# Performance work log

Measured on AMD Instinct MI355X. Metric: run time of the kernel, lower is better.

The kernel has to match this reference:

```python
import jax, jax.numpy as jnp
import numpy as np

B, S, IN, HID, HEADS, TRAITS = 128, 32, 32, 128, 8, 10


def setup_inputs() -> dict:
    key = jax.random.key(0)
    ks = jax.random.split(key, 40)
    f32 = jnp.float32
    def W(k, shape, s=0.02):
        return (jax.random.normal(k, shape, f32) * s)
    path = jax.random.normal(ks[0], (B, S, IN), f32)
    # monotonically increasing shared time grid (timestamps[0] is what cdeint uses)
    dt = jax.random.uniform(ks[1], (S,), f32, 0.05, 0.15)
    ts = jnp.broadcast_to(jnp.cumsum(dt), (B, S))
    inp = {
        "interaction_path": path,
        "timestamps": ts,
        # initial encoder: Linear(IN,HID) -> LN -> GELU -> Linear(HID,HID) -> LN
        "enc_W1": W(ks[2], (IN, HID)), "enc_b1": jnp.zeros((HID,), f32),
        "enc_g1": jnp.ones((HID,), f32), "enc_bt1": jnp.zeros((HID,), f32),
        "enc_W2": W(ks[3], (HID, HID)), "enc_b2": jnp.zeros((HID,), f32),
        "enc_g2": jnp.ones((HID,), f32), "enc_bt2": jnp.zeros((HID,), f32),
        # vector field: Linear(HID,2HID)->LN->GELU -> Linear(2HID,2HID)->LN->GELU -> Linear(2HID,HID*IN)
        "vf_W1": W(ks[4], (HID, 2 * HID)), "vf_b1": jnp.zeros((2 * HID,), f32),
        "vf_g1": jnp.ones((2 * HID,), f32), "vf_bt1": jnp.zeros((2 * HID,), f32),
        "vf_W2": W(ks[5], (2 * HID, 2 * HID)), "vf_b2": jnp.zeros((2 * HID,), f32),
        "vf_g2": jnp.ones((2 * HID,), f32), "vf_bt2": jnp.zeros((2 * HID,), f32),
        "vf_W3": W(ks[6], (2 * HID, HID * IN), 0.005), "vf_b3": jnp.zeros((HID * IN,), f32),
        # MultiheadAttention (q=k=v, single token)
        "Wq": W(ks[7], (HID, HID)), "bq": jnp.zeros((HID,), f32),
        "Wk": W(ks[8], (HID, HID)), "bk": jnp.zeros((HID,), f32),
        "Wv": W(ks[9], (HID, HID)), "bv": jnp.zeros((HID,), f32),
        "Wo": W(ks[10], (HID, HID)), "bo": jnp.zeros((HID,), f32),
        # trait decoder (2-layer MLP -> TRAITS)
        "dec_W1": W(ks[11], (HID, HID)), "dec_b1": jnp.zeros((HID,), f32),
        "dec_W2": W(ks[12], (HID, TRAITS)), "dec_b2": jnp.zeros((TRAITS,), f32),
    }
    return inp


def reference(interaction_path, timestamps,
              enc_W1, enc_b1, enc_g1, enc_bt1, enc_W2, enc_b2, enc_g2, enc_bt2,
              vf_W1, vf_b1, vf_g1, vf_bt1, vf_W2, vf_b2, vf_g2, vf_bt2, vf_W3, vf_b3,
              Wq, bq, Wk, bk, Wv, bv, Wo, bo,
              dec_W1, dec_b1, dec_W2, dec_b2):
    b, s, in_dim = interaction_path.shape
    hid = enc_W1.shape[1]
    nh = HEADS
    dh = hid // nh

    def ln(x, g, bb):
        mu = jnp.mean(x, -1, keepdims=True)
        v = jnp.mean((x - mu) ** 2, -1, keepdims=True)
        return (x - mu) / jnp.sqrt(v + 1e-5) * g + bb

    gelu = lambda x: jax.nn.gelu(x, approximate=False)

    # initial encoder on first time point (dropout = eval mode)
    x0 = interaction_path[:, 0]
    h0 = gelu(ln(x0 @ enc_W1 + enc_b1, enc_g1, enc_bt1))
    z0 = ln(h0 @ enc_W2 + enc_b2, enc_g2, enc_bt2)  # [B, HID]

    # linear-interpolation control path: piecewise-constant derivative per interval
    dts = timestamps[:, 1:] - timestamps[:, :-1]                       # [B, S-1]
    dX = (interaction_path[:, 1:] - interaction_path[:, :-1]) / dts[..., None]  # [B, S-1, IN]

    def vf(z):
        h = gelu(ln(z @ vf_W1 + vf_b1, vf_g1, vf_bt1))
        h = gelu(ln(h @ vf_W2 + vf_b2, vf_g2, vf_bt2))
        return (h @ vf_W3 + vf_b3).reshape(z.shape[0], hid, in_dim)    # [B, HID, IN]

    def drift(z, dxdt):
        return jnp.einsum('bhi,bi->bh', vf(z), dxdt)

    def rk4_step(z, inp):
        dxdt, hstep = inp               # [B, IN], [B]
        hb = hstep[:, None]
        k1 = drift(z, dxdt)
        k2 = drift(z + 0.5 * hb * k1, dxdt)
        k3 = drift(z + 0.5 * hb * k2, dxdt)
        k4 = drift(z + hb * k3, dxdt)
        z_next = z + (hb / 6.0) * (k1 + 2 * k2 + 2 * k3 + k4)
        return z_next, None

    zT, _ = jax.lax.scan(rk4_step, z0, (jnp.swapaxes(dX, 0, 1), dts.T))  # [B, HID]

    # single-token self-attention (softmax over one key -> weights = 1)
    q = (zT @ Wq + bq).reshape(b, nh, dh)
    k = (zT @ Wk + bk).reshape(b, nh, dh)
    v = (zT @ Wv + bv).reshape(b, nh, dh)
    scores = jnp.sum(q * k, -1, keepdims=True) / jnp.sqrt(jnp.float32(dh))  # [B, nh, 1]
    w = jax.nn.softmax(scores[..., None], axis=-1)                           # [B, nh, 1, 1] == 1
    attn = (w[..., 0] * v).reshape(b, hid)
    final = attn @ Wo + bo
    attention_weights = jnp.mean(w, axis=1)  # [B, 1, 1] averaged over heads (torch default)

    hD = gelu(final @ dec_W1 + dec_b1)
    traits = hD @ dec_W2 + dec_b2            # [B, TRAITS]
    return traits, attention_weights
```

## Files before the change

kernel.cpp:

```cpp
#include <hip/hip_runtime.h>
#include <hip/hip_bf16.h>

#define BB 128
#define SS 32
#define NSTEP 31
#define IND 32
#define HID 128
#define HID2 256

typedef unsigned short u16;
typedef unsigned int u32;
typedef _Float16 f16;
typedef f16 h2 __attribute__((ext_vector_type(2)));
typedef __fp16 fp16v2 __attribute__((ext_vector_type(2)));
typedef _Float16 f16x8 __attribute__((ext_vector_type(8)));
typedef float f32x4 __attribute__((ext_vector_type(4)));

__device__ __forceinline__ float dot2f(u32 a, u32 b, float c){
#if __has_builtin(__builtin_amdgcn_fdot2)
  h2 ha, hb; __builtin_memcpy(&ha, &a, 4); __builtin_memcpy(&hb, &b, 4);
  return __builtin_amdgcn_fdot2(ha, hb, c, false);
#else
  h2 ha, hb; __builtin_memcpy(&ha, &a, 4); __builtin_memcpy(&hb, &b, 4);
  return c + (float)ha[0]*(float)hb[0] + (float)ha[1]*(float)hb[1];
#endif
}
__device__ __forceinline__ u32 pkh2(float a, float b){
  fp16v2 r = __builtin_amdgcn_cvt_pkrtz(a, b);
  u32 u; __builtin_memcpy(&u, &r, 4); return u;
}
__device__ __forceinline__ u16 f2h(float f){ f16 h = (f16)f; u16 u; __builtin_memcpy(&u, &h, 2); return u; }
__device__ __forceinline__ float gelu_f(float x){ return 0.5f * x * (1.0f + erff(x * 0.70710678118654752440f)); }

__device__ __forceinline__ float wred(float v){
  int iv; float tf;
  #define DPPADD(CTRL, RMASK) \
    __builtin_memcpy(&iv, &v, 4); \
    iv = __builtin_amdgcn_update_dpp(0, iv, CTRL, RMASK, 0xf, true); \
    __builtin_memcpy(&tf, &iv, 4); \
    v += tf;
  DPPADD(0x111, 0xf)
  DPPADD(0x112, 0xf)
  DPPADD(0x114, 0xf)
  DPPADD(0x118, 0xf)
  DPPADD(0x142, 0xa)
  DPPADD(0x143, 0xc)
  #undef DPPADD
  return v;
}

__device__ __forceinline__ void bsum2(float x, float y, float* red, int tid, float& ox, float& oy){
  #pragma unroll
  for (int off = 32; off >= 1; off >>= 1){ x += __shfl_xor(x, off); y += __shfl_xor(y, off); }
  __syncthreads();
  if ((tid & 63) == 0){ red[(tid >> 6)*2] = x; red[(tid >> 6)*2 + 1] = y; }
  __syncthreads();
  ox = red[0] + red[2] + red[4] + red[6];
  oy = red[1] + red[3] + red[5] + red[7];
}

__global__ __launch_bounds__(128) void prep_misc(const float* __restrict__ path,
                                                 const float* __restrict__ ts,
                                                 const float* __restrict__ b3,
                                                 u32* __restrict__ dxh,
                                                 float* __restrict__ hb,
                                                 float* __restrict__ gb){
  const int b = blockIdx.x, tid = threadIdx.x;
  __shared__ float sdx[NSTEP * IND];
  for (int t = tid; t < NSTEP * IND; t += 128){
    int s = t >> 5, i = t & 31;
    float dt = ts[b*SS + s + 1] - ts[b*SS + s];
    sdx[t] = (path[(b*SS + s + 1)*IND + i] - path[(b*SS + s)*IND + i]) / dt;
  }
  if (tid < NSTEP) hb[b*NSTEP + tid] = ts[b*SS + tid + 1] - ts[b*SS + tid];
  __syncthreads();
  for (int t = tid; t < NSTEP * 16; t += 128){
    int s = t >> 4, i2 = t & 15;
    dxh[((size_t)b*NSTEP + s)*16 + i2] = pkh2(sdx[s*IND + 2*i2], sdx[s*IND + 2*i2 + 1]);
  }
  if (tid < HID){
    float w[IND];
    #pragma unroll
    for (int i = 0; i < IND; ++i) w[i] = b3[tid*IND + i];
    for (int s = 0; s < NSTEP; ++s){
      float a = 0.f;
      #pragma unroll
      for (int i = 0; i < IND; ++i) a = fmaf(w[i], sdx[s*IND + i], a);
      gb[(b*NSTEP + s)*HID + tid] = a;
    }
  }
}

__global__ __launch_bounds__(256) void pack_w3(const float* __restrict__ W3, u32* __restrict__ w3h){
  int i = blockIdx.x*256 + threadIdx.x;
  if (i < (HID2*HID*IND)/2) w3h[i] = pkh2(W3[2*i], W3[2*i + 1]);
}

__global__ __launch_bounds__(256) void pack_wf(const float* __restrict__ W1,
                                               const float* __restrict__ W2,
                                               u32* __restrict__ w1f,
                                               u32* __restrict__ w2f){
  int i = blockIdx.x*256 + threadIdx.x;
  if (i < 16384){
    int lane_blk = i >> 6, rem = i & 63;
    int i16 = rem >> 2, q = rem & 3;
    int w = lane_blk >> 6, lane = lane_blk & 63;
    int kt = i16 >> 2, nt = i16 & 3;
    int k = kt*32 + (lane >> 4)*8 + 2*q;
    int col = w*64 + nt*16 + (lane & 15);
    w1f[i] = pkh2(W1[(size_t)k*HID2 + col], W1[(size_t)(k+1)*HID2 + col]);
  } else if (i < 16384 + 32768){
    int j = i - 16384;
    int lane_blk = j >> 7, rem = j & 127;
    int i32i = rem >> 2, q = rem & 3;
    int w = lane_blk >> 6, lane = lane_blk & 63;
    int kt = i32i >> 2, nt = i32i & 3;
    int k = kt*32 + (lane >> 4)*8 + 2*q;
    int col = w*64 + nt*16 + (lane & 15);
    w2f[j] = pkh2(W2[(size_t)k*HID2 + col], W2[(size_t)(k+1)*HID2 + col]);
  }
}

__global__ __launch_bounds__(256) void gprep_h(const u32* __restrict__ w3h,
                                               const u32* __restrict__ dxh,
                                               u32* __restrict__ Gp, int s0){
  const int tid = threadIdx.x;
  const int sl = blockIdx.y; const int s = s0 + sl;
  const int lin = blockIdx.x*256 + tid;
  const int kp = lin >> 7, h = lin & 127;
  const uint4* wa = (const uint4*)(w3h + ((size_t)(2*kp)*HID + h)*16);
  const uint4* wb = (const uint4*)(w3h + ((size_t)(2*kp+1)*HID + h)*16);
  uint4 A0 = wa[0], A1 = wa[1], A2 = wa[2], A3 = wa[3];
  uint4 B0 = wb[0], B1 = wb[1], B2 = wb[2], B3 = wb[3];
  __shared__ u32 sdx[BB * 16];
  for (int t = tid; t < BB * 16; t += 256){
    int bb = t >> 4, i2 = t & 15;
    sdx[t] = dxh[((size_t)bb*NSTEP + s)*16 + i2];
  }
  __syncthreads();
  const int kt = kp >> 4, q = kp & 3, quad2 = (kp >> 2) & 3;
  const int wq = h >> 5, tq = (h >> 4) & 1, nn = h & 15;
  const size_t off = (size_t)wq*4096 + (size_t)(kt*2 + tq)*256 + (size_t)(quad2*16 + nn)*4 + q;
  const size_t base_sl = (size_t)sl * BB * 16384;
  for (int bb = 0; bb < BB; ++bb){
    const uint4* dp = (const uint4*)&sdx[bb*16];
    uint4 D0 = dp[0], D1 = dp[1], D2 = dp[2], D3 = dp[3];
    float g0 = 0.f, g1 = 0.f, g2 = 0.f, g3 = 0.f;
    g0 = dot2f(D0.x, A0.x, g0); g0 = dot2f(D0.y, A0.y, g0);
    g0 = dot2f(D0.z, A0.z, g0); g0 = dot2f(D0.w, A0.w, g0);
    g2 = dot2f(D1.x, A1.x, g2); g2 = dot2f(D1.y, A1.y, g2);
    g2 = dot2f(D1.z, A1.z, g2); g2 = dot2f(D1.w, A1.w, g2);
    g0 = dot2f(D2.x, A2.x, g0); g0 = dot2f(D2.y, A2.y, g0);
    g0 = dot2f(D2.z, A2.z, g0); g0 = dot2f(D2.w, A2.w, g0);
    g2 = dot2f(D3.x, A3.x, g2); g2 = dot2f(D3.y, A3.y, g2);
    g2 = dot2f(D3.z, A3.z, g2); g2 = dot2f(D3.w, A3.w, g2);
    g1 = dot2f(D0.x, B0.x, g1); g1 = dot2f(D0.y, B0.y, g1);
    g1 = dot2f(D0.z, B0.z, g1); g1 = dot2f(D0.w, B0.w, g1);
    g3 = dot2f(D1.x, B1.x, g3); g3 = dot2f(D1.y, B1.y, g3);
    g3 = dot2f(D1.z, B1.z, g3); g3 = dot2f(D1.w, B1.w, g3);
    g1 = dot2f(D2.x, B2.x, g1); g1 = dot2f(D2.y, B2.y, g1);
    g1 = dot2f(D2.z, B2.z, g1); g1 = dot2f(D2.w, B2.w, g1);
    g3 = dot2f(D3.x, B3.x, g3); g3 = dot2f(D3.y, B3.y, g3);
    g3 = dot2f(D3.z, B3.z, g3); g3 = dot2f(D3.w, B3.w, g3);
    Gp[base_sl + (size_t)bb*16384 + off] = pkh2(g0 + g2, g1 + g3);
  }
}

struct ScanP {
  const float *path;
  const float *eW1,*eb1,*eg1,*ebt1,*eW2,*eb2,*eg2,*ebt2;
  const u32 *w1f, *w2f;
  const float *b1,*g1,*bt1,*b2,*g2,*bt2;
  const float *Wv,*bv,*Wo,*bo,*dW1,*db1,*dW2,*db2;
  const float *hb,*gb;
  const u32 *Gp;
  float *zstate, *out;
  int s0, s1, do_enc, do_epi;
};

__global__ __launch_bounds__(256, 1) void scan_kernel(ScanP p){
  const int tid = threadIdx.x;
  const int b = blockIdx.x;
  const int lane = tid & 63, w = tid >> 6;
  const int quad = lane >> 4, n16 = lane & 15;
  const bool owner = (quad == 0);
  __shared__ __align__(16) u16 zst_h[HID];
  __shared__ __align__(16) u16 a1p_h[HID2];
  __shared__ __align__(16) u16 a2p_h[HID2];
  __shared__ __align__(16) float red[8];
  __shared__ __align__(16) float zf[HID];
  __shared__ __align__(16) float sc1[HID2];

  uint4 w1r[16], w2r[32];
  {
    const uint4* s1p = (const uint4*)p.w1f + ((size_t)(w*64 + lane))*16;
    #pragma unroll
    for (int i = 0; i < 16; ++i) w1r[i] = s1p[i];
    const uint4* s2p = (const uint4*)p.w2f + ((size_t)(w*64 + lane))*32;
    #pragma unroll
    for (int i = 0; i < 32; ++i) w2r[i] = s2p[i];
  }
  float rb1[4], rg1[4], rbt1[4], rb2[4], rg2[4], rbt2[4];
  #pragma unroll
  for (int nt = 0; nt < 4; ++nt){
    int col = w*64 + nt*16 + n16;
    rb1[nt] = p.b1[col]; rg1[nt] = p.g1[col]; rbt1[nt] = p.bt1[col];
    rb2[nt] = p.b2[col]; rg2[nt] = p.g2[col]; rbt2[nt] = p.bt2[col];
  }
  const int h0 = w*32 + n16, h1 = h0 + 16;

  float mu, sq;
  if (p.do_enc){
    if (tid < IND) sc1[tid] = p.path[(b*SS + 0)*IND + tid];
    __syncthreads();
    float acc = 0.f;
    if (tid < HID){
      acc = p.eb1[tid];
      #pragma unroll 8
      for (int i = 0; i < IND; ++i) acc = fmaf(sc1[i], p.eW1[i*HID + tid], acc);
    }
    float cx = (tid < HID) ? acc : 0.f;
    bsum2(cx, cx*cx, red, tid, mu, sq);
    mu *= (1.f/HID); float var = sq*(1.f/HID) - mu*mu; float rstd = rsqrtf(var + 1e-5f);
    if (tid < HID) zf[tid] = gelu_f((acc - mu)*rstd*p.eg1[tid] + p.ebt1[tid]);
    __syncthreads();
    float acc2 = 0.f;
    if (tid < HID){
      acc2 = p.eb2[tid];
      #pragma unroll 8
      for (int h = 0; h < HID; ++h) acc2 = fmaf(zf[h], p.eW2[h*HID + tid], acc2);
    }
    cx = (tid < HID) ? acc2 : 0.f;
    bsum2(cx, cx*cx, red, tid, mu, sq);
    mu *= (1.f/HID); float var2 = sq*(1.f/HID) - mu*mu; float rstd2 = rsqrtf(var2 + 1e-5f);
    __syncthreads();
    if (tid < HID) zf[tid] = (acc2 - mu)*rstd2*p.eg2[tid] + p.ebt2[tid];
    __syncthreads();
  }
  float zc0 = 0.f, zc1 = 0.f;
  if (owner){
    if (p.do_enc){ zc0 = zf[h0]; zc1 = zf[h1]; }
    else { zc0 = p.zstate[b*HID + h0]; zc1 = p.zstate[b*HID + h1]; }
  }

  for (int s = p.s0; s < p.s1; ++s){
    const float hbv = p.hb[b*NSTEP + s];
    uint4 gr[16];
    {
      const uint4* g4 = (const uint4*)(p.Gp + ((size_t)(s - p.s0)*BB + b)*16384 + (size_t)w*4096);
      #pragma unroll
      for (int m = 0; m < 16; ++m) gr[m] = g4[m*64 + lane];
    }
    float gb0 = 0.f, gb1 = 0.f;
    if (owner){
      gb0 = p.gb[(b*NSTEP + s)*HID + h0];
      gb1 = p.gb[(b*NSTEP + s)*HID + h1];
      zst_h[h0] = f2h(zc0); zst_h[h1] = f2h(zc1);
    }
    float ks0 = 0.f, ks1 = 0.f;
    __syncthreads();

    #pragma unroll 1
    for (int st = 0; st < 4; ++st){
      f32x4 D0 = {0,0,0,0}, D1 = {0,0,0,0}, D2 = {0,0,0,0}, D3 = {0,0,0,0};
      {
        const uint4* za = (const uint4*)zst_h;
        #pragma unroll
        for (int kt = 0; kt < 4; ++kt){
          f16x8 a; uint4 av = za[kt*4 + quad]; __builtin_memcpy(&a, &av, 16);
          f16x8 bf;
          __builtin_memcpy(&bf, &w1r[kt*4+0], 16); D0 = __builtin_amdgcn_mfma_f32_16x16x32_f16(a, bf, D0, 0, 0, 0);
          __builtin_memcpy(&bf, &w1r[kt*4+1], 16); D1 = __builtin_amdgcn_mfma_f32_16x16x32_f16(a, bf, D1, 0, 0, 0);
          __builtin_memcpy(&bf, &w1r[kt*4+2], 16); D2 = __builtin_amdgcn_mfma_f32_16x16x32_f16(a, bf, D2, 0, 0, 0);
          __builtin_memcpy(&bf, &w1r[kt*4+3], 16); D3 = __builtin_amdgcn_mfma_f32_16x16x32_f16(a, bf, D3, 0, 0, 0);
        }
      }
      float v0 = D0[0] + rb1[0], v1 = D1[0] + rb1[1], v2 = D2[0] + rb1[2], v3 = D3[0] + rb1[3];
      float ssum = wred((v0 + v1) + (v2 + v3));
      float ssq  = wred((v0*v0 + v1*v1) + (v2*v2 + v3*v3));
      if (lane == 63){ red[w*2] = ssum; red[w*2+1] = ssq; }
      __syncthreads();
      {
        const float4* r4 = (const float4*)red;
        float4 ra = r4[0], rb = r4[1];
        float m1 = (ra.x + ra.z + rb.x + rb.z)*(1.f/1024.f);
        float q1 = (ra.y + ra.w + rb.y + rb.w)*(1.f/1024.f);
        float rs1 = rsqrtf(q1 - m1*m1 + 1e-5f);
        if (owner){
          a1p_h[w*64 +  0 + n16] = f2h(gelu_f((v0 - m1)*rs1*rg1[0] + rbt1[0]));
          a1p_h[w*64 + 16 + n16] = f2h(gelu_f((v1 - m1)*rs1*rg1[1] + rbt1[1]));
          a1p_h[w*64 + 32 + n16] = f2h(gelu_f((v2 - m1)*rs1*rg1[2] + rbt1[2]));
          a1p_h[w*64 + 48 + n16] = f2h(gelu_f((v3 - m1)*rs1*rg1[3] + rbt1[3]));
        }
      }
      __syncthreads();
      D0 = {0,0,0,0}; D1 = {0,0,0,0}; D2 = {0,0,0,0}; D3 = {0,0,0,0};
      {
        const uint4* aa = (const uint4*)a1p_h;
        #pragma unroll
        for (int kt = 0; kt < 8; ++kt){
          f16x8 a; uint4 av = aa[kt*4 + quad]; __builtin_memcpy(&a, &av, 16);
          f16x8 bf;
          __builtin_memcpy(&bf, &w2r[kt*4+0], 16); D0 = __builtin_amdgcn_mfma_f32_16x16x32_f16(a, bf, D0, 0, 0, 0);
          __builtin_memcpy(&bf, &w2r[kt*4+1], 16); D1 = __builtin_amdgcn_mfma_f32_16x16x32_f16(a, bf, D1, 0, 0, 0);
          __builtin_memcpy(&bf, &w2r[kt*4+2], 16); D2 = __builtin_amdgcn_mfma_f32_16x16x32_f16(a, bf, D2, 0, 0, 0);
          __builtin_memcpy(&bf, &w2r[kt*4+3], 16); D3 = __builtin_amdgcn_mfma_f32_16x16x32_f16(a, bf, D3, 0, 0, 0);
        }
      }
      v0 = D0[0] + rb2[0]; v1 = D1[0] + rb2[1]; v2 = D2[0] + rb2[2]; v3 = D3[0] + rb2[3];
      ssum = wred((v0 + v1) + (v2 + v3));
      ssq  = wred((v0*v0 + v1*v1) + (v2*v2 + v3*v3));
      if (lane == 63){ red[w*2] = ssum; red[w*2+1] = ssq; }
      __syncthreads();
      {
        const float4* r4 = (const float4*)red;
        float4 ra = r4[0], rb = r4[1];
        float m2 = (ra.x + ra.z + rb.x + rb.z)*(1.f/1024.f);
        float q2 = (ra.y + ra.w + rb.y + rb.w)*(1.f/1024.f);
        float rs2 = rsqrtf(q2 - m2*m2 + 1e-5f);
        if (owner){
          a2p_h[w*64 +  0 + n16] = f2h(gelu_f((v0 - m2)*rs2*rg2[0] + rbt2[0]));
          a2p_h[w*64 + 16 + n16] = f2h(gelu_f((v1 - m2)*rs2*rg2[1] + rbt2[1]));
          a2p_h[w*64 + 32 + n16] = f2h(gelu_f((v2 - m2)*rs2*rg2[2] + rbt2[2]));
          a2p_h[w*64 + 48 + n16] = f2h(gelu_f((v3 - m2)*rs2*rg2[3] + rbt2[3]));
        }
      }
      __syncthreads();
      f32x4 E0 = {0,0,0,0}, E1 = {0,0,0,0};
      {
        const uint4* aa = (const uint4*)a2p_h;
        #pragma unroll
        for (int kt = 0; kt < 8; ++kt){
          f16x8 a; uint4 av = aa[kt*4 + quad]; __builtin_memcpy(&a, &av, 16);
          f16x8 g0f, g1f;
          __builtin_memcpy(&g0f, &gr[kt*2+0], 16);
          __builtin_memcpy(&g1f, &gr[kt*2+1], 16);
          E0 = __builtin_amdgcn_mfma_f32_16x16x32_f16(a, g0f, E0, 0, 0, 0);
          E1 = __builtin_amdgcn_mfma_f32_16x16x32_f16(a, g1f, E1, 0, 0, 0);
        }
      }
      if (owner){
        float kv0 = E0[0] + gb0, kv1 = E1[0] + gb1;
        float cst = (st == 0 || st == 3) ? 1.f : 2.f;
        ks0 += cst*kv0; ks1 += cst*kv1;
        if (st < 3){
          float c = (st == 2) ? hbv : 0.5f*hbv;
          zst_h[h0] = f2h(zc0 + c*kv0);
          zst_h[h1] = f2h(zc1 + c*kv1);
        }
      }
      __syncthreads();
    }
    if (owner){ zc0 += hbv*(1.f/6.f)*ks0; zc1 += hbv*(1.f/6.f)*ks1; }
  }

  if (p.do_epi){
    if (owner){ zf[h0] = zc0; zf[h1] = zc1; }
    __syncthreads();
    if (tid < HID){
      float v = p.bv[tid];
      #pragma unroll 8
      for (int h = 0; h < HID; ++h) v = fmaf(zf[h], p.Wv[h*HID + tid], v);
      sc1[tid] = v;
    }
    __syncthreads();
    if (tid < HID){
      float f = p.bo[tid];
      #pragma unroll 8
      for (int h = 0; h < HID; ++h) f = fmaf(sc1[h], p.Wo[h*HID + tid], f);
      sc1[HID + tid] = f;
    }
    __syncthreads();
    if (tid < HID){
      float hd = p.db1[tid];
      #pragma unroll 8
      for (int h = 0; h < HID; ++h) hd = fmaf(sc1[HID + h], p.dW1[h*HID + tid], hd);
      zf[tid] = gelu_f(hd);
    }
    __syncthreads();
    if (tid < 10){
      float t = p.db2[tid];
      #pragma unroll 8
      for (int h = 0; h < HID; ++h) t = fmaf(zf[h], p.dW2[h*10 + tid], t);
      p.out[b*10 + tid] = t;
    }
    if (tid == 0) p.out[BB*10 + b] = 1.0f;
  } else {
    if (owner){ p.zstate[b*HID + h0] = zc0; p.zstate[b*HID + h1] = zc1; }
  }
}

extern "C" void kernel_launch(void* const* d_in, const int* in_sizes, int n_in,
                              void* d_out, int out_size, void* d_ws, size_t ws_size,
                              hipStream_t stream){
  const float* path  = (const float*)d_in[0];
  const float* ts    = (const float*)d_in[1];
  const float* eW1   = (const float*)d_in[2];
  const float* eb1   = (const float*)d_in[3];
  const float* eg1   = (const float*)d_in[4];
  const float* ebt1  = (const float*)d_in[5];
  const float* eW2   = (const float*)d_in[6];
  const float* eb2   = (const float*)d_in[7];
  const float* eg2   = (const float*)d_in[8];
  const float* ebt2  = (const float*)d_in[9];
  const float* vW1   = (const float*)d_in[10];
  const float* vb1   = (const float*)d_in[11];
  const float* vg1   = (const float*)d_in[12];
  const float* vbt1  = (const float*)d_in[13];
  const float* vW2   = (const float*)d_in[14];
  const float* vb2   = (const float*)d_in[15];
  const float* vg2   = (const float*)d_in[16];
  const float* vbt2  = (const float*)d_in[17];
  const float* vW3   = (const float*)d_in[18];
  const float* vb3   = (const float*)d_in[19];
  const float* Wv    = (const float*)d_in[24];
  const float* bv    = (const float*)d_in[25];
  const float* Wo    = (const float*)d_in[26];
  const float* bo    = (const float*)d_in[27];
  const float* dW1   = (const float*)d_in[28];
  const float* db1   = (const float*)d_in[29];
  const float* dW2   = (const float*)d_in[30];
  const float* db2   = (const float*)d_in[31];

  char* wsb = (char*)d_ws;
  float* z_state = (float*)(wsb + 0);
  u32*   dxh = (u32*)(wsb + 65536);
  float* hb  = (float*)(wsb + 319488);
  float* gb  = (float*)(wsb + 335872);
  u32*   w3h = (u32*)(wsb + 2367488);
  u32*   w1f = (u32*)(wsb + 4464640);
  u32*   w2f = (u32*)(wsb + 4530176);
  u32*   Gp  = (u32*)(wsb + 4661248);

  hipLaunchKernelGGL(prep_misc, dim3(BB), dim3(128), 0, stream, path, ts, vb3, dxh, hb, gb);
  hipLaunchKernelGGL(pack_w3, dim3(2048), dim3(256), 0, stream, vW3, w3h);
  hipLaunchKernelGGL(pack_wf, dim3(192), dim3(256), 0, stream, vW1, vW2, w1f, w2f);

  const size_t per_step = (size_t)BB * 16384 * 4;
  size_t gav = (ws_size > 4661248) ? (ws_size - 4661248) : per_step;
  int chunk = (int)(gav / per_step);
  if (chunk < 1) chunk = 1;
  if (chunk > NSTEP) chunk = NSTEP;

  for (int s0 = 0; s0 < NSTEP; s0 += chunk){
    int cs = (NSTEP - s0 < chunk) ? (NSTEP - s0) : chunk;
    hipLaunchKernelGGL(gprep_h, dim3(64, cs), dim3(256), 0, stream, w3h, dxh, Gp, s0);
    ScanP P;
    P.path = path;
    P.eW1 = eW1; P.eb1 = eb1; P.eg1 = eg1; P.ebt1 = ebt1;
    P.eW2 = eW2; P.eb2 = eb2; P.eg2 = eg2; P.ebt2 = ebt2;
    P.w1f = w1f; P.w2f = w2f;
    P.b1 = vb1; P.g1 = vg1; P.bt1 = vbt1;
    P.b2 = vb2; P.g2 = vg2; P.bt2 = vbt2;
    P.Wv = Wv; P.bv = bv; P.Wo = Wo; P.bo = bo;
    P.dW1 = dW1; P.db1 = db1; P.dW2 = dW2; P.db2 = db2;
    P.hb = hb; P.gb = gb; P.Gp = Gp;
    P.zstate = z_state; P.out = (float*)d_out;
    P.s0 = s0; P.s1 = s0 + cs;
    P.do_enc = (s0 == 0) ? 1 : 0;
    P.do_epi = (s0 + cs == NSTEP) ? 1 : 0;
    hipLaunchKernelGGL(scan_kernel, dim3(BB), dim3(256), 0, stream, P);
  }
}
```

Before: 608.6 us.

## Overlap G precompute of next chunk with scan of current chunk in fused launch

Merges the gprep and scan kernels into one kernel that, in each launch, runs the RK4 scan for chunk i on the first 128 blocks and precomputes the G tensor for chunk i+1 on extra blocks. G is double-buffered in the workspace. The goal is to fill idle CUs during the latency-bound scan (only 128 blocks) with the bandwidth-heavy G prep. It also caps chunk size at 8 steps, which adds more launches, and shared memory grows for the scan blocks because both paths are compiled into one kernel.

```diff
diff --git a/kernel.cpp b/kernel.cpp
--- a/kernel.cpp
+++ b/kernel.cpp
@@ -66,17 +66,17 @@
                                                  float* __restrict__ hb,
                                                  float* __restrict__ gb){
   const int b = blockIdx.x, tid = threadIdx.x;
-  __shared__ float sdx[NSTEP * IND];
+  __shared__ float sdxp[NSTEP * IND];
   for (int t = tid; t < NSTEP * IND; t += 128){
     int s = t >> 5, i = t & 31;
     float dt = ts[b*SS + s + 1] - ts[b*SS + s];
-    sdx[t] = (path[(b*SS + s + 1)*IND + i] - path[(b*SS + s)*IND + i]) / dt;
+    sdxp[t] = (path[(b*SS + s + 1)*IND + i] - path[(b*SS + s)*IND + i]) / dt;
   }
   if (tid < NSTEP) hb[b*NSTEP + tid] = ts[b*SS + tid + 1] - ts[b*SS + tid];
   __syncthreads();
   for (int t = tid; t < NSTEP * 16; t += 128){
     int s = t >> 4, i2 = t & 15;
-    dxh[((size_t)b*NSTEP + s)*16 + i2] = pkh2(sdx[s*IND + 2*i2], sdx[s*IND + 2*i2 + 1]);
+    dxh[((size_t)b*NSTEP + s)*16 + i2] = pkh2(sdxp[s*IND + 2*i2], sdxp[s*IND + 2*i2 + 1]);
   }
   if (tid < HID){
     float w[IND];
@@ -85,7 +85,7 @@
     for (int s = 0; s < NSTEP; ++s){
       float a = 0.f;
       #pragma unroll
-      for (int i = 0; i < IND; ++i) a = fmaf(w[i], sdx[s*IND + i], a);
+      for (int i = 0; i < IND; ++i) a = fmaf(w[i], sdxp[s*IND + i], a);
       gb[(b*NSTEP + s)*HID + tid] = a;
     }
   }
@@ -121,52 +121,7 @@
   }
 }
 
-__global__ __launch_bounds__(256) void gprep_h(const u32* __restrict__ w3h,
-                                               const u32* __restrict__ dxh,
-                                               u32* __restrict__ Gp, int s0){
-  const int tid = threadIdx.x;
-  const int sl = blockIdx.y; const int s = s0 + sl;
-  const int lin = blockIdx.x*256 + tid;
-  const int kp = lin >> 7, h = lin & 127;
-  const uint4* wa = (const uint4*)(w3h + ((size_t)(2*kp)*HID + h)*16);
-  const uint4* wb = (const uint4*)(w3h + ((size_t)(2*kp+1)*HID + h)*16);
-  uint4 A0 = wa[0], A1 = wa[1], A2 = wa[2], A3 = wa[3];
-  uint4 B0 = wb[0], B1 = wb[1], B2 = wb[2], B3 = wb[3];
-  __shared__ u32 sdx[BB * 16];
-  for (int t = tid; t < BB * 16; t += 256){
-    int bb = t >> 4, i2 = t & 15;
-    sdx[t] = dxh[((size_t)bb*NSTEP + s)*16 + i2];
-  }
-  __syncthreads();
-  const int kt = kp >> 4, q = kp & 3, quad2 = (kp >> 2) & 3;
-  const int wq = h >> 5, tq = (h >> 4) & 1, nn = h & 15;
-  const size_t off = (size_t)wq*4096 + (size_t)(kt*2 + tq)*256 + (size_t)(quad2*16 + nn)*4 + q;
-  const size_t base_sl = (size_t)sl * BB * 16384;
-  for (int bb = 0; bb < BB; ++bb){
-    const uint4* dp = (const uint4*)&sdx[bb*16];
-    uint4 D0 = dp[0], D1 = dp[1], D2 = dp[2], D3 = dp[3];
-    float g0 = 0.f, g1 = 0.f, g2 = 0.f, g3 = 0.f;
-    g0 = dot2f(D0.x, A0.x, g0); g0 = dot2f(D0.y, A0.y, g0);
-    g0 = dot2f(D0.z, A0.z, g0); g0 = dot2f(D0.w, A0.w, g0);
-    g2 = dot2f(D1.x, A1.x, g2); g2 = dot2f(D1.y, A1.y, g2);
-    g2 = dot2f(D1.z, A1.z, g2); g2 = dot2f(D1.w, A1.w, g2);
-    g0 = dot2f(D2.x, A2.x, g0); g0 = dot2f(D2.y, A2.y, g0);
-    g0 = dot2f(D2.z, A2.z, g0); g0 = dot2f(D2.w, A2.w, g0);
-    g2 = dot2f(D3.x, A3.x, g2); g2 = dot2f(D3.y, A3.y, g2);
-    g2 = dot2f(D3.z, A3.z, g2); g2 = dot2f(D3.w, A3.w, g2);
-    g1 = dot2f(D0.x, B0.x, g1); g1 = dot2f(D0.y, B0.y, g1);
-    g1 = dot2f(D0.z, B0.z, g1); g1 = dot2f(D0.w, B0.w, g1);
-    g3 = dot2f(D1.x, B1.x, g3); g3 = dot2f(D1.y, B1.y, g3);
-    g3 = dot2f(D1.z, B1.z, g3); g3 = dot2f(D1.w, B1.w, g3);
-    g1 = dot2f(D2.x, B2.x, g1); g1 = dot2f(D2.y, B2.y, g1);
-    g1 = dot2f(D2.z, B2.z, g1); g1 = dot2f(D2.w, B2.w, g1);
-    g3 = dot2f(D3.x, B3.x, g3); g3 = dot2f(D3.y, B3.y, g3);
-    g3 = dot2f(D3.z, B3.z, g3); g3 = dot2f(D3.w, B3.w, g3);
-    Gp[base_sl + (size_t)bb*16384 + off] = pkh2(g0 + g2, g1 + g3);
-  }
-}
-
-struct ScanP {
+struct FusedP {
   const float *path;
   const float *eW1,*eb1,*eg1,*ebt1,*eW2,*eb2,*eg2,*ebt2;
   const u32 *w1f, *w2f;
@@ -175,218 +130,271 @@
   const float *hb,*gb;
   const u32 *Gp;
   float *zstate, *out;
-  int s0, s1, do_enc, do_epi;
+  int s0, s1, do_enc, do_epi, scan_on;
+  const u32 *w3h, *dxh;
+  u32 *Gpw;
+  int ps0, pcs;
 };
 
-__global__ __launch_bounds__(256, 1) void scan_kernel(ScanP p){
+__global__ __launch_bounds__(256, 1) void fused_kernel(FusedP p){
   const int tid = threadIdx.x;
-  const int b = blockIdx.x;
-  const int lane = tid & 63, w = tid >> 6;
-  const int quad = lane >> 4, n16 = lane & 15;
-  const bool owner = (quad == 0);
   __shared__ __align__(16) u16 zst_h[HID];
   __shared__ __align__(16) u16 a1p_h[HID2];
   __shared__ __align__(16) u16 a2p_h[HID2];
   __shared__ __align__(16) float red[8];
   __shared__ __align__(16) float zf[HID];
   __shared__ __align__(16) float sc1[HID2];
-
-  uint4 w1r[16], w2r[32];
+  __shared__ u32 sdx[BB * 16];
+
+  if (p.scan_on && blockIdx.x < BB){
+    const int b = blockIdx.x;
+    const int lane = tid & 63, w = tid >> 6;
+    const int quad = lane >> 4, n16 = lane & 15;
+    const bool owner = (quad == 0);
+
+    uint4 w1r[16], w2r[32];
+    {
+      const uint4* s1p = (const uint4*)p.w1f + ((size_t)(w*64 + lane))*16;
+      #pragma unroll
+      for (int i = 0; i < 16; ++i) w1r[i] = s1p[i];
+      const uint4* s2p = (const uint4*)p.w2f + ((size_t)(w*64 + lane))*32;
+      #pragma unroll
+      for (int i = 0; i < 32; ++i) w2r[i] = s2p[i];
+    }
+    float rb1[4], rg1[4], rbt1[4], rb2[4], rg2[4], rbt2[4];
+    #pragma unroll
+    for (int nt = 0; nt < 4; ++nt){
+      int col = w*64 + nt*16 + n16;
+      rb1[nt] = p.b1[col]; rg1[nt] = p.g1[col]; rbt1[nt] = p.bt1[col];
+      rb2[nt] = p.b2[col]; rg2[nt] = p.g2[col]; rbt2[nt] = p.bt2[col];
+    }
+    const int h0 = w*32 + n16, h1 = h0 + 16;
+
+    float mu, sq;
+    if (p.do_enc){
+      if (tid < IND) sc1[tid] = p.path[(b*SS + 0)*IND + tid];
+      __syncthreads();
+      float acc = 0.f;
+      if (tid < HID){
+        acc = p.eb1[tid];
+        #pragma unroll 8
+        for (int i = 0; i < IND; ++i) acc = fmaf(sc1[i], p.eW1[i*HID + tid], acc);
+      }
+      float cx = (tid < HID) ? acc : 0.f;
+      bsum2(cx, cx*cx, red, tid, mu, sq);
+      mu *= (1.f/HID); float var = sq*(1.f/HID) - mu*mu; float rstd = rsqrtf(var + 1e-5f);
+      if (tid < HID) zf[tid] = gelu_f((acc - mu)*rstd*p.eg1[tid] + p.ebt1[tid]);
+      __syncthreads();
+      float acc2 = 0.f;
+      if (tid < HID){
+        acc2 = p.eb2[tid];
+        #pragma unroll 8
+        for (int h = 0; h < HID; ++h) acc2 = fmaf(zf[h], p.eW2[h*HID + tid], acc2);
+      }
+      cx = (tid < HID) ? acc2 : 0.f;
+      bsum2(cx, cx*cx, red, tid, mu, sq);
+      mu *= (1.f/HID); float var2 = sq*(1.f/HID) - mu*mu; float rstd2 = rsqrtf(var2 + 1e-5f);
+      __syncthreads();
+      if (tid < HID) zf[tid] = (acc2 - mu)*rstd2*p.eg2[tid] + p.ebt2[tid];
+      __syncthreads();
+    }
+    float zc0 = 0.f, zc1 = 0.f;
+    if (owner){
+      if (p.do_enc){ zc0 = zf[h0]; zc1 = zf[h1]; }
+      else { zc0 = p.zstate[b*HID + h0]; zc1 = p.zstate[b*HID + h1]; }
+    }
+
+    for (int s = p.s0; s < p.s1; ++s){
+      const float hbv = p.hb[b*NSTEP + s];
+      uint4 gr[16];
+      {
+        const uint4* g4 = (const uint4*)(p.Gp + ((size_t)(s - p.s0)*BB + b)*16384 + (size_t)w*4096);
+        #pragma unroll
+        for (int m = 0; m < 16; ++m) gr[m] = g4[m*64 + lane];
+      }
+      float gb0 = 0.f, gb1 = 0.f;
+      if (owner){
+        gb0 = p.gb[(b*NSTEP + s)*HID + h0];
+        gb1 = p.gb[(b*NSTEP + s)*HID + h1];
+        zst_h[h0] = f2h(zc0); zst_h[h1] = f2h(zc1);
+      }
+      float ks0 = 0.f, ks1 = 0.f;
+      __syncthreads();
+
+      #pragma unroll 1
+      for (int st = 0; st < 4; ++st){
+        f32x4 D0 = {0,0,0,0}, D1 = {0,0,0,0}, D2 = {0,0,0,0}, D3 = {0,0,0,0};
+        {
+          const uint4* za = (const uint4*)zst_h;
+          #pragma unroll
+          for (int kt = 0; kt < 4; ++kt){
+            f16x8 a; uint4 av = za[kt*4 + quad]; __builtin_memcpy(&a, &av, 16);
+            f16x8 bf;
+            __builtin_memcpy(&bf, &w1r[kt*4+0], 16); D0 = __builtin_amdgcn_mfma_f32_16x16x32_f16(a, bf, D0, 0, 0, 0);
+            __builtin_memcpy(&bf, &w1r[kt*4+1], 16); D1 = __builtin_amdgcn_mfma_f32_16x16x32_f16(a, bf, D1, 0, 0, 0);
+            __builtin_memcpy(&bf, &w1r[kt*4+2], 16); D2 = __builtin_amdgcn_mfma_f32_16x16x32_f16(a, bf, D2, 0, 0, 0);
+            __builtin_memcpy(&bf, &w1r[kt*4+3], 16); D3 = __builtin_amdgcn_mfma_f32_16x16x32_f16(a, bf, D3, 0, 0, 0);
+          }
+        }
+        float v0 = D0[0] + rb1[0], v1 = D1[0] + rb1[1], v2 = D2[0] + rb1[2], v3 = D3[0] + rb1[3];
+        float ssum = wred((v0 + v1) + (v2 + v3));
+        float ssq  = wred((v0*v0 + v1*v1) + (v2*v2 + v3*v3));
+        if (lane == 63){ red[w*2] = ssum; red[w*2+1] = ssq; }
+        __syncthreads();
+        {
+          const float4* r4 = (const float4*)red;
+          float4 ra = r4[0], rb = r4[1];
+          float m1 = (ra.x + ra.z + rb.x + rb.z)*(1.f/1024.f);
+          float q1 = (ra.y + ra.w + rb.y + rb.w)*(1.f/1024.f);
+          float rs1 = rsqrtf(q1 - m1*m1 + 1e-5f);
+          if (owner){
+            a1p_h[w*64 +  0 + n16] = f2h(gelu_f((v0 - m1)*rs1*rg1[0] + rbt1[0]));
+            a1p_h[w*64 + 16 + n16] = f2h(gelu_f((v1 - m1)*rs1*rg1[1] + rbt1[1]));
+            a1p_h[w*64 + 32 + n16] = f2h(gelu_f((v2 - m1)*rs1*rg1[2] + rbt1[2]));
+            a1p_h[w*64 + 48 + n16] = f2h(gelu_f((v3 - m1)*rs1*rg1[3] + rbt1[3]));
+          }
+        }
+        __syncthreads();
+        D0 = {0,0,0,0}; D1 = {0,0,0,0}; D2 = {0,0,0,0}; D3 = {0,0,0,0};
+        {
+          const uint4* aa = (const uint4*)a1p_h;
+          #pragma unroll
+          for (int kt = 0; kt < 8; ++kt){
+            f16x8 a; uint4 av = aa[kt*4 + quad]; __builtin_memcpy(&a, &av, 16);
+            f16x8 bf;
+            __builtin_memcpy(&bf, &w2r[kt*4+0], 16); D0 = __builtin_amdgcn_mfma_f32_16x16x32_f16(a, bf, D0, 0, 0, 0);
+            __builtin_memcpy(&bf, &w2r[kt*4+1], 16); D1 = __builtin_amdgcn_mfma_f32_16x16x32_f16(a, bf, D1, 0, 0, 0);
+            __builtin_memcpy(&bf, &w2r[kt*4+2], 16); D2 = __builtin_amdgcn_mfma_f32_16x16x32_f16(a, bf, D2, 0, 0, 0);
+            __builtin_memcpy(&bf, &w2r[kt*4+3], 16); D3 = __builtin_amdgcn_mfma_f32_16x16x32_f16(a, bf, D3, 0, 0, 0);
+          }
+        }
+        v0 = D0[0] + rb2[0]; v1 = D1[0] + rb2[1]; v2 = D2[0] + rb2[2]; v3 = D3[0] + rb2[3];
+        ssum = wred((v0 + v1) + (v2 + v3));
+        ssq  = wred((v0*v0 + v1*v1) + (v2*v2 + v3*v3));
+        if (lane == 63){ red[w*2] = ssum; red[w*2+1] = ssq; }
+        __syncthreads();
+        {
+          const float4* r4 = (const float4*)red;
+          float4 ra = r4[0], rb = r4[1];
+          float m2 = (ra.x + ra.z + rb.x + rb.z)*(1.f/1024.f);
+          float q2 = (ra.y + ra.w + rb.y + rb.w)*(1.f/1024.f);
+          float rs2 = rsqrtf(q2 - m2*m2 + 1e-5f);
+          if (owner){
+            a2p_h[w*64 +  0 + n16] = f2h(gelu_f((v0 - m2)*rs2*rg2[0] + rbt2[0]));
+            a2p_h[w*64 + 16 + n16] = f2h(gelu_f((v1 - m2)*rs2*rg2[1] + rbt2[1]));
+            a2p_h[w*64 + 32 + n16] = f2h(gelu_f((v2 - m2)*rs2*rg2[2] + rbt2[2]));
+            a2p_h[w*64 + 48 + n16] = f2h(gelu_f((v3 - m2)*rs2*rg2[3] + rbt2[3]));
+          }
+        }
+        __syncthreads();
+        f32x4 E0 = {0,0,0,0}, E1 = {0,0,0,0};
+        {
+          const uint4* aa = (const uint4*)a2p_h;
+          #pragma unroll
+          for (int kt = 0; kt < 8; ++kt){
+            f16x8 a; uint4 av = aa[kt*4 + quad]; __builtin_memcpy(&a, &av, 16);
+            f16x8 g0f, g1f;
+            __builtin_memcpy(&g0f, &gr[kt*2+0], 16);
+            __builtin_memcpy(&g1f, &gr[kt*2+1], 16);
+            E0 = __builtin_amdgcn_mfma_f32_16x16x32_f16(a, g0f, E0, 0, 0, 0);
+            E1 = __builtin_amdgcn_mfma_f32_16x16x32_f16(a, g1f, E1, 0, 0, 0);
+          }
+        }
+        if (owner){
+          float kv0 = E0[0] + gb0, kv1 = E1[0] + gb1;
+          float cst = (st == 0 || st == 3) ? 1.f : 2.f;
+          ks0 += cst*kv0; ks1 += cst*kv1;
+          if (st < 3){
+            float c = (st == 2) ? hbv : 0.5f*hbv;
+            zst_h[h0] = f2h(zc0 + c*kv0);
+            zst_h[h1] = f2h(zc1 + c*kv1);
+          }
+        }
+        __syncthreads();
+      }
+      if (owner){ zc0 += hbv*(1.f/6.f)*ks0; zc1 += hbv*(1.f/6.f)*ks1; }
+    }
+
+    if (p.do_epi){
+      if (owner){ zf[h0] = zc0; zf[h1] = zc1; }
+      __syncthreads();
+      if (tid < HID){
+        float v = p.bv[tid];
+        #pragma unroll 8
+        for (int h = 0; h < HID; ++h) v = fmaf(zf[h], p.Wv[h*HID + tid], v);
+        sc1[tid] = v;
+      }
+      __syncthreads();
+      if (tid < HID){
+        float f = p.bo[tid];
+        #pragma unroll 8
+        for (int h = 0; h < HID; ++h) f = fmaf(sc1[h], p.Wo[h*HID + tid], f);
+        sc1[HID + tid] = f;
+      }
+      __syncthreads();
+      if (tid < HID){
+        float hd = p.db1[tid];
+        #pragma unroll 8
+        for (int h = 0; h < HID; ++h) hd = fmaf(sc1[HID + h], p.dW1[h*HID + tid], hd);
+        zf[tid] = gelu_f(hd);
+      }
+      __syncthreads();
+      if (tid < 10){
+        float t = p.db2[tid];
+        #pragma unroll 8
+        for (int h = 0; h < HID; ++h) t = fmaf(zf[h], p.dW2[h*10 + tid], t);
+        p.out[b*10 + tid] = t;
+      }
+      if (tid == 0) p.out[BB*10 + b] = 1.0f;
+    } else {
+      if (owner){ p.zstate[b*HID + h0] = zc0; p.zstate[b*HID + h1] = zc1; }
+    }
+    return;
+  }
+
   {
-    const uint4* s1p = (const uint4*)p.w1f + ((size_t)(w*64 + lane))*16;
-    #pragma unroll
-    for (int i = 0; i < 16; ++i) w1r[i] = s1p[i];
-    const uint4* s2p = (const uint4*)p.w2f + ((size_t)(w*64 + lane))*32;
-    #pragma unroll
-    for (int i = 0; i < 32; ++i) w2r[i] = s2p[i];
-  }
-  float rb1[4], rg1[4], rbt1[4], rb2[4], rg2[4], rbt2[4];
-  #pragma unroll
-  for (int nt = 0; nt < 4; ++nt){
-    int col = w*64 + nt*16 + n16;
-    rb1[nt] = p.b1[col]; rg1[nt] = p.g1[col]; rbt1[nt] = p.bt1[col];
-    rb2[nt] = p.b2[col]; rg2[nt] = p.g2[col]; rbt2[nt] = p.bt2[col];
-  }
-  const int h0 = w*32 + n16, h1 = h0 + 16;
-
-  float mu, sq;
-  if (p.do_enc){
-    if (tid < IND) sc1[tid] = p.path[(b*SS + 0)*IND + tid];
+    const int pb = blockIdx.x - (p.scan_on ? BB : 0);
+    const int sl = pb >> 6, xblk = pb & 63;
+    if (sl >= p.pcs) return;
+    const int s = p.ps0 + sl;
+    const int lin = xblk*256 + tid;
+    const int kp = lin >> 7, h = lin & 127;
+    const uint4* wa = (const uint4*)(p.w3h + ((size_t)(2*kp)*HID + h)*16);
+    const uint4* wb = (const uint4*)(p.w3h + ((size_t)(2*kp+1)*HID + h)*16);
+    uint4 A0 = wa[0], A1 = wa[1], A2 = wa[2], A3 = wa[3];
+    uint4 B0 = wb[0], B1 = wb[1], B2 = wb[2], B3 = wb[3];
+    for (int t = tid; t < BB * 16; t += 256){
+      int bb = t >> 4, i2 = t & 15;
+      sdx[t] = p.dxh[((size_t)bb*NSTEP + s)*16 + i2];
+    }
     __syncthreads();
-    float acc = 0.f;
-    if (tid < HID){
-      acc = p.eb1[tid];
-      #pragma unroll 8
-      for (int i = 0; i < IND; ++i) acc = fmaf(sc1[i], p.eW1[i*HID + tid], acc);
-    }
-    float cx = (tid < HID) ? acc : 0.f;
-    bsum2(cx, cx*cx, red, tid, mu, sq);
-    mu *= (1.f/HID); float var = sq*(1.f/HID) - mu*mu; float rstd = rsqrtf(var + 1e-5f);
-    if (tid < HID) zf[tid] = gelu_f((acc - mu)*rstd*p.eg1[tid] + p.ebt1[tid]);
-    __syncthreads();
-    float acc2 = 0.f;
-    if (tid < HID){
-      acc2 = p.eb2[tid];
-      #pragma unroll 8
-      for (int h = 0; h < HID; ++h) acc2 = fmaf(zf[h], p.eW2[h*HID + tid], acc2);
-    }
-    cx = (tid < HID) ? acc2 : 0.f;
-    bsum2(cx, cx*cx, red, tid, mu, sq);
-    mu *= (1.f/HID); float var2 = sq*(1.f/HID) - mu*mu; float rstd2 = rsqrtf(var2 + 1e-5f);
-    __syncthreads();
-    if (tid < HID) zf[tid] = (acc2 - mu)*rstd2*p.eg2[tid] + p.ebt2[tid];
-    __syncthreads();
-  }
-  float zc0 = 0.f, zc1 = 0.f;
-  if (owner){
-    if (p.do_enc){ zc0 = zf[h0]; zc1 = zf[h1]; }
-    else { zc0 = p.zstate[b*HID + h0]; zc1 = p.zstate[b*HID + h1]; }
-  }
-
-  for (int s = p.s0; s < p.s1; ++s){
-    const float hbv = p.hb[b*NSTEP + s];
-    uint4 gr[16];
-    {
-      const uint4* g4 = (const uint4*)(p.Gp + ((size_t)(s - p.s0)*BB + b)*16384 + (size_t)w*4096);
-      #pragma unroll
-      for (int m = 0; m < 16; ++m) gr[m] = g4[m*64 + lane];
-    }
-    float gb0 = 0.f, gb1 = 0.f;
-    if (owner){
-      gb0 = p.gb[(b*NSTEP + s)*HID + h0];
-      gb1 = p.gb[(b*NSTEP + s)*HID + h1];
-      zst_h[h0] = f2h(zc0); zst_h[h1] = f2h(zc1);
-    }
-    float ks0 = 0.f, ks1 = 0.f;
-    __syncthreads();
-
-    #pragma unroll 1
-    for (int st = 0; st < 4; ++st){
-      f32x4 D0 = {0,0,0,0}, D1 = {0,0,0,0}, D2 = {0,0,0,0}, D3 = {0,0,0,0};
-      {
-        const uint4* za = (const uint4*)zst_h;
-        #pragma unroll
-        for (int kt = 0; kt < 4; ++kt){
-          f16x8 a; uint4 av = za[kt*4 + quad]; __builtin_memcpy(&a, &av, 16);
-          f16x8 bf;
-          __builtin_memcpy(&bf, &w1r[kt*4+0], 16); D0 = __builtin_amdgcn_mfma_f32_16x16x32_f16(a, bf, D0, 0, 0, 0);
-          __builtin_memcpy(&bf, &w1r[kt*4+1], 16); D1 = __builtin_amdgcn_mfma_f32_16x16x32_f16(a, bf, D1, 0, 0, 0);
-          __builtin_memcpy(&bf, &w1r[kt*4+2], 16); D2 = __builtin_amdgcn_mfma_f32_16x16x32_f16(a, bf, D2, 0, 0, 0);
-          __builtin_memcpy(&bf, &w1r[kt*4+3], 16); D3 = __builtin_amdgcn_mfma_f32_16x16x32_f16(a, bf, D3, 0, 0, 0);
-        }
-      }
-      float v0 = D0[0] + rb1[0], v1 = D1[0] + rb1[1], v2 = D2[0] + rb1[2], v3 = D3[0] + rb1[3];
-      float ssum = wred((v0 + v1) + (v2 + v3));
-      float ssq  = wred((v0*v0 + v1*v1) + (v2*v2 + v3*v3));
-      if (lane == 63){ red[w*2] = ssum; red[w*2+1] = ssq; }
-      __syncthreads();
-      {
-        const float4* r4 = (const float4*)red;
-        float4 ra = r4[0], rb = r4[1];
-        float m1 = (ra.x + ra.z + rb.x + rb.z)*(1.f/1024.f);
-        float q1 = (ra.y + ra.w + rb.y + rb.w)*(1.f/1024.f);
-        float rs1 = rsqrtf(q1 - m1*m1 + 1e-5f);
-        if (owner){
-          a1p_h[w*64 +  0 + n16] = f2h(gelu_f((v0 - m1)*rs1*rg1[0] + rbt1[0]));
-          a1p_h[w*64 + 16 + n16] = f2h(gelu_f((v1 - m1)*rs1*rg1[1] + rbt1[1]));
-          a1p_h[w*64 + 32 + n16] = f2h(gelu_f((v2 - m1)*rs1*rg1[2] + rbt1[2]));
-          a1p_h[w*64 + 48 + n16] = f2h(gelu_f((v3 - m1)*rs1*rg1[3] + rbt1[3]));
-        }
-      }
-      __syncthreads();
-      D0 = {0,0,0,0}; D1 = {0,0,0,0}; D2 = {0,0,0,0}; D3 = {0,0,0,0};
-      {
-        const uint4* aa = (const uint4*)a1p_h;
-        #pragma unroll
-        for (int kt = 0; kt < 8; ++kt){
-          f16x8 a; uint4 av = aa[kt*4 + quad]; __builtin_memcpy(&a, &av, 16);
-          f16x8 bf;
-          __builtin_memcpy(&bf, &w2r[kt*4+0], 16); D0 = __builtin_amdgcn_mfma_f32_16x16x32_f16(a, bf, D0, 0, 0, 0);
-          __builtin_memcpy(&bf, &w2r[kt*4+1], 16); D1 = __builtin_amdgcn_mfma_f32_16x16x32_f16(a, bf, D1, 0, 0, 0);
-          __builtin_memcpy(&bf, &w2r[kt*4+2], 16); D2 = __builtin_amdgcn_mfma_f32_16x16x32_f16(a, bf, D2, 0, 0, 0);
-          __builtin_memcpy(&bf, &w2r[kt*4+3], 16); D3 = __builtin_amdgcn_mfma_f32_16x16x32_f16(a, bf, D3, 0, 0, 0);
-        }
-      }
-      v0 = D0[0] + rb2[0]; v1 = D1[0] + rb2[1]; v2 = D2[0] + rb2[2]; v3 = D3[0] + rb2[3];
-      ssum = wred((v0 + v1) + (v2 + v3));
-      ssq  = wred((v0*v0 + v1*v1) + (v2*v2 + v3*v3));
-      if (lane == 63){ red[w*2] = ssum; red[w*2+1] = ssq; }
-      __syncthreads();
-      {
-        const float4* r4 = (const float4*)red;
-        float4 ra = r4[0], rb = r4[1];
-        float m2 = (ra.x + ra.z + rb.x + rb.z)*(1.f/1024.f);
-        float q2 = (ra.y + ra.w + rb.y + rb.w)*(1.f/1024.f);
-        float rs2 = rsqrtf(q2 - m2*m2 + 1e-5f);
-        if (owner){
-          a2p_h[w*64 +  0 + n16] = f2h(gelu_f((v0 - m2)*rs2*rg2[0] + rbt2[0]));
-          a2p_h[w*64 + 16 + n16] = f2h(gelu_f((v1 - m2)*rs2*rg2[1] + rbt2[1]));
-          a2p_h[w*64 + 32 + n16] = f2h(gelu_f((v2 - m2)*rs2*rg2[2] + rbt2[2]));
-          a2p_h[w*64 + 48 + n16] = f2h(gelu_f((v3 - m2)*rs2*rg2[3] + rbt2[3]));
-        }
-      }
-      __syncthreads();
-      f32x4 E0 = {0,0,0,0}, E1 = {0,0,0,0};
-      {
-        const uint4* aa = (const uint4*)a2p_h;
-        #pragma unroll
-        for (int kt = 0; kt < 8; ++kt){
-          f16x8 a; uint4 av = aa[kt*4 + quad]; __builtin_memcpy(&a, &av, 16);
-          f16x8 g0f, g1f;
-          __builtin_memcpy(&g0f, &gr[kt*2+0], 16);
-          __builtin_memcpy(&g1f, &gr[kt*2+1], 16);
-          E0 = __builtin_amdgcn_mfma_f32_16x16x32_f16(a, g0f, E0, 0, 0, 0);
-          E1 = __builtin_amdgcn_mfma_f32_16x16x32_f16(a, g1f, E1, 0, 0, 0);
-        }
-      }
-      if (owner){
-        float kv0 = E0[0] + gb0, kv1 = E1[0] + gb1;
-        float cst = (st == 0 || st == 3) ? 1.f : 2.f;
-        ks0 += cst*kv0; ks1 += cst*kv1;
-        if (st < 3){
-          float c = (st == 2) ? hbv : 0.5f*hbv;
-          zst_h[h0] = f2h(zc0 + c*kv0);
-          zst_h[h1] = f2h(zc1 + c*kv1);
-        }
-      }
-      __syncthreads();
-    }
-    if (owner){ zc0 += hbv*(1.f/6.f)*ks0; zc1 += hbv*(1.f/6.f)*ks1; }
-  }
-
-  if (p.do_epi){
-    if (owner){ zf[h0] = zc0; zf[h1] = zc1; }
-    __syncthreads();
-    if (tid < HID){
-      float v = p.bv[tid];
-      #pragma unroll 8
-      for (int h = 0; h < HID; ++h) v = fmaf(zf[h], p.Wv[h*HID + tid], v);
-      sc1[tid] = v;
-    }
-    __syncthreads();
-    if (tid < HID){
-      float f = p.bo[tid];
-      #pragma unroll 8
-      for (int h = 0; h < HID; ++h) f = fmaf(sc1[h], p.Wo[h*HID + tid], f);
-      sc1[HID + tid] = f;
-    }
-    __syncthreads();
-    if (tid < HID){
-      float hd = p.db1[tid];
-      #pragma unroll 8
-      for (int h = 0; h < HID; ++h) hd = fmaf(sc1[HID + h], p.dW1[h*HID + tid], hd);
-      zf[tid] = gelu_f(hd);
-    }
-    __syncthreads();
-    if (tid < 10){
-      float t = p.db2[tid];
-      #pragma unroll 8
-      for (int h = 0; h < HID; ++h) t = fmaf(zf[h], p.dW2[h*10 + tid], t);
-      p.out[b*10 + tid] = t;
-    }
-    if (tid == 0) p.out[BB*10 + b] = 1.0f;
-  } else {
-    if (owner){ p.zstate[b*HID + h0] = zc0; p.zstate[b*HID + h1] = zc1; }
+    const int kt = kp >> 4, q = kp & 3, quad2 = (kp >> 2) & 3;
+    const int wq = h >> 5, tq = (h >> 4) & 1, nn = h & 15;
+    const size_t off = (size_t)wq*4096 + (size_t)(kt*2 + tq)*256 + (size_t)(quad2*16 + nn)*4 + q;
+    const size_t base_sl = (size_t)sl * BB * 16384;
+    u32* __restrict__ Gout = p.Gpw;
+    for (int bb = 0; bb < BB; ++bb){
+      const uint4* dp = (const uint4*)&sdx[bb*16];
+      uint4 D0 = dp[0], D1 = dp[1], D2 = dp[2], D3 = dp[3];
+      float g0 = 0.f, g1 = 0.f, g2 = 0.f, g3 = 0.f;
+      g0 = dot2f(D0.x, A0.x, g0); g0 = dot2f(D0.y, A0.y, g0);
+      g0 = dot2f(D0.z, A0.z, g0); g0 = dot2f(D0.w, A0.w, g0);
+      g2 = dot2f(D1.x, A1.x, g2); g2 = dot2f(D1.y, A1.y, g2);
+      g2 = dot2f(D1.z, A1.z, g2); g2 = dot2f(D1.w, A1.w, g2);
+      g0 = dot2f(D2.x, A2.x, g0); g0 = dot2f(D2.y, A2.y, g0);
+      g0 = dot2f(D2.z, A2.z, g0); g0 = dot2f(D2.w, A2.w, g0);
+      g2 = dot2f(D3.x, A3.x, g2); g2 = dot2f(D3.y, A3.y, g2);
+      g2 = dot2f(D3.z, A3.z, g2); g2 = dot2f(D3.w, A3.w, g2);
+      g1 = dot2f(D0.x, B0.x, g1); g1 = dot2f(D0.y, B0.y, g1);
+      g1 = dot2f(D0.z, B0.z, g1); g1 = dot2f(D0.w, B0.w, g1);
+      g3 = dot2f(D1.x, B1.x, g3); g3 = dot2f(D1.y, B1.y, g3);
+      g3 = dot2f(D1.z, B1.z, g3); g3 = dot2f(D1.w, B1.w, g3);
+      g1 = dot2f(D2.x, B2.x, g1); g1 = dot2f(D2.y, B2.y, g1);
+      g1 = dot2f(D2.z, B2.z, g1); g1 = dot2f(D2.w, B2.w, g1);
+      g3 = dot2f(D3.x, B3.x, g3); g3 = dot2f(D3.y, B3.y, g3);
+      g3 = dot2f(D3.z, B3.z, g3); g3 = dot2f(D3.w, B3.w, g3);
+      Gout[base_sl + (size_t)bb*16384 + off] = pkh2(g0 + g2, g1 + g3);
+    }
   }
 }
 
@@ -430,35 +438,82 @@
   u32*   w3h = (u32*)(wsb + 2367488);
   u32*   w1f = (u32*)(wsb + 4464640);
   u32*   w2f = (u32*)(wsb + 4530176);
-  u32*   Gp  = (u32*)(wsb + 4661248);
+  const size_t gbase = 4661248;
 
   hipLaunchKernelGGL(prep_misc, dim3(BB), dim3(128), 0, stream, path, ts, vb3, dxh, hb, gb);
   hipLaunchKernelGGL(pack_w3, dim3(2048), dim3(256), 0, stream, vW3, w3h);
   hipLaunchKernelGGL(pack_wf, dim3(192), dim3(256), 0, stream, vW1, vW2, w1f, w2f);
 
   const size_t per_step = (size_t)BB * 16384 * 4;
-  size_t gav = (ws_size > 4661248) ? (ws_size - 4661248) : per_step;
-  int chunk = (int)(gav / per_step);
-  if (chunk < 1) chunk = 1;
-  if (chunk > NSTEP) chunk = NSTEP;
-
-  for (int s0 = 0; s0 < NSTEP; s0 += chunk){
-    int cs = (NSTEP - s0 < chunk) ? (NSTEP - s0) : chunk;
-    hipLaunchKernelGGL(gprep_h, dim3(64, cs), dim3(256), 0, stream, w3h, dxh, Gp, s0);
-    ScanP P;
-    P.path = path;
-    P.eW1 = eW1; P.eb1 = eb1; P.eg1 = eg1; P.ebt1 = ebt1;
-    P.eW2 = eW2; P.eb2 = eb2; P.eg2 = eg2; P.ebt2 = ebt2;
-    P.w1f = w1f; P.w2f = w2f;
-    P.b1 = vb1; P.g1 = vg1; P.bt1 = vbt1;
-    P.b2 = vb2; P.g2 = vg2; P.bt2 = vbt2;
-    P.Wv = Wv; P.bv = bv; P.Wo = Wo; P.bo = bo;
-    P.dW1 = dW1; P.db1 = db1; P.dW2 = dW2; P.db2 = db2;
-    P.hb = hb; P.gb = gb; P.Gp = Gp;
-    P.zstate = z_state; P.out = (float*)d_out;
-    P.s0 = s0; P.s1 = s0 + cs;
-    P.do_enc = (s0 == 0) ? 1 : 0;
-    P.do_epi = (s0 + cs == NSTEP) ? 1 : 0;
-    hipLaunchKernelGGL(scan_kernel, dim3(BB), dim3(256), 0, stream, P);
-  }
-}
+  size_t avail = (ws_size > gbase) ? (ws_size - gbase) : 0;
+  int pipelined, c;
+  int capp = (int)((avail/2) / per_step);
+  if (capp >= 2){
+    pipelined = 1;
+    c = capp < 8 ? capp : 8;
+    if (c > NSTEP) c = NSTEP;
+  } else {
+    pipelined = 0;
+    c = (int)(avail / per_step);
+    if (c < 1) c = 1;
+    if (c > NSTEP) c = NSTEP;
+  }
+  const int nch = (NSTEP + c - 1) / c;
+  u32* GpA = (u32*)(wsb + gbase);
+  u32* GpB = (u32*)(wsb + gbase + (size_t)c*per_step);
+
+  FusedP base;
+  base.path = path;
+  base.eW1 = eW1; base.eb1 = eb1; base.eg1 = eg1; base.ebt1 = ebt1;
+  base.eW2 = eW2; base.eb2 = eb2; base.eg2 = eg2; base.ebt2 = ebt2;
+  base.w1f = w1f; base.w2f = w2f;
+  base.b1 = vb1; base.g1 = vg1; base.bt1 = vbt1;
+  base.b2 = vb2; base.g2 = vg2; base.bt2 = vbt2;
+  base.Wv = Wv; base.bv = bv; base.Wo = Wo; base.bo = bo;
+  base.dW1 = dW1; base.db1 = db1; base.dW2 = dW2; base.db2 = db2;
+  base.hb = hb; base.gb = gb;
+  base.zstate = z_state; base.out = (float*)d_out;
+  base.w3h = w3h; base.dxh = dxh;
+  base.Gp = GpA; base.Gpw = GpA;
+  base.s0 = 0; base.s1 = 0; base.do_enc = 0; base.do_epi = 0; base.scan_on = 0;
+  base.ps0 = 0; base.pcs = 0;
+
+  if (pipelined){
+    for (int i = 0; i <= nch; ++i){
+      FusedP P = base;
+      int scan_i = i - 1, prep_i = i;
+      P.scan_on = (scan_i >= 0) ? 1 : 0;
+      if (P.scan_on){
+        P.s0 = scan_i*c;
+        P.s1 = (P.s0 + c < NSTEP) ? (P.s0 + c) : NSTEP;
+        P.Gp = (scan_i & 1) ? GpB : GpA;
+        P.do_enc = (scan_i == 0) ? 1 : 0;
+        P.do_epi = (P.s1 == NSTEP) ? 1 : 0;
+      }
+      if (prep_i < nch){
+        P.ps0 = prep_i*c;
+        P.pcs = (NSTEP - P.ps0 < c) ? (NSTEP - P.ps0) : c;
+        P.Gpw = (prep_i & 1) ? GpB : GpA;
+      } else {
+        P.pcs = 0;
+      }
+      int grid = (P.scan_on ? BB : 0) + 64*P.pcs;
+      if (grid == 0) continue;
+      hipLaunchKernelGGL(fused_kernel, dim3(grid), dim3(256), 0, stream, P);
+    }
+  } else {
+    for (int i = 0; i < nch; ++i){
+      int s0 = i*c;
+      int cs = (NSTEP - s0 < c) ? (NSTEP - s0) : c;
+      FusedP P1 = base;
+      P1.scan_on = 0; P1.ps0 = s0; P1.pcs = cs; P1.Gpw = GpA;
+      hipLaunchKernelGGL(fused_kernel, dim3(64*cs), dim3(256), 0, stream, P1);
+      FusedP P2 = base;
+      P2.scan_on = 1; P2.pcs = 0;
+      P2.s0 = s0; P2.s1 = s0 + cs; P2.Gp = GpA;
+      P2.do_enc = (s0 == 0) ? 1 : 0;
+      P2.do_epi = (s0 + cs == NSTEP) ? 1 : 0;
+      hipLaunchKernelGGL(fused_kernel, dim3(BB), dim3(256), 0, stream, P2);
+    }
+  }
+}
```

Measured after the change: 541.8 us. -11.0%, faster.
